# Performance work log

Hardware: AMD Instinct MI355X
Metric: run time of the kernel (lower is better)

## Reference

```python
import jax, jax.numpy as jnp
import numpy as np

N, S, D, H, L = 1024, 128, 128, 4, 2  # nodes, seq_len, d_model(=heads*C), heads, layers
C = D // H
EPS = 1e-5


def _bn(x, g, b):
    # torch BatchNorm1d training mode applied to [N, D, S]: per-channel stats over (node, seq)
    m = x.mean(axis=(0, 1))
    v = x.var(axis=(0, 1))  # biased variance, matching torch BN normalization
    return (x - m) * jax.lax.rsqrt(v + EPS) * g + b


def _ln(x, g, b):
    m = x.mean(-1, keepdims=True)
    v = x.var(-1, keepdims=True)
    return (x - m) * jax.lax.rsqrt(v + EPS) * g + b


def setup_inputs() -> dict:
    key = jax.random.key(0)
    ks = jax.random.split(key, 16)
    w = lambda k, shape: (jax.random.normal(k, shape, jnp.float32) * 0.05)
    x = jax.random.normal(ks[0], (N, S, D), jnp.float32)
    pad_mask = (jax.random.uniform(ks[1], (N, S, S)) > 0.2).astype(jnp.float32)
    ones = lambda shape: jnp.ones(shape, jnp.float32)
    zeros = lambda shape: jnp.zeros(shape, jnp.float32)
    inp = {
        'x': x, 'pad_mask': pad_mask,
        'lin_in_W': w(ks[2], (D, D)), 'lin_in_b': zeros((D,)),
        'in_bn_g': ones((D,)), 'in_bn_b': zeros((D,)),
        'q_W': w(ks[3], (L, D, D)), 'q_b': zeros((L, D)),
        'q_bn_g': ones((L, D)), 'q_bn_b': zeros((L, D)),
        'k_W': w(ks[4], (L, D, D)), 'k_b': zeros((L, D)),
        'k_bn_g': ones((L, D)), 'k_bn_b': zeros((L, D)),
        'v_W': w(ks[5], (L, D, D)), 'v_b': zeros((L, D)),
        'v_bn_g': ones((L, D)), 'v_bn_b': zeros((L, D)),
        'ln_g': ones((L, D)), 'ln_b': zeros((L, D)),
        'ff_W': w(ks[6], (L, D, D)), 'ff_b': zeros((L, D)),
        'ff_bn_g': ones((L, D)), 'ff_bn_b': zeros((L, D)),
        'skip_W': w(ks[7], (L, D, D)), 'skip_b': zeros((L, D)),
        'skip_bn_g': ones((L, D)), 'skip_bn_b': zeros((L, D)),
    }
    return inp


def reference(x, pad_mask, lin_in_W, lin_in_b, in_bn_g, in_bn_b,
              q_W, q_b, q_bn_g, q_bn_b, k_W, k_b, k_bn_g, k_bn_b,
              v_W, v_b, v_bn_g, v_bn_b, ln_g, ln_b,
              ff_W, ff_b, ff_bn_g, ff_bn_b, skip_W, skip_b, skip_bn_g, skip_bn_b):
    # DetourTransformer.forward: lin_in -> in_bn -> L DetourTransformerLayers -> take seq position 0
    h = _bn(x @ lin_in_W.T + lin_in_b, in_bn_g, in_bn_b)
    mask = pad_mask[:, None]  # [N,1,S,S], multiplicative mask applied BEFORE softmax
    for l in range(L):
        q = _bn(h @ q_W[l].T + q_b[l], q_bn_g[l], q_bn_b[l]).reshape(N, S, H, C)
        k = _bn(h @ k_W[l].T + k_b[l], k_bn_g[l], k_bn_b[l]).reshape(N, S, H, C)
        v = _bn(h @ v_W[l].T + v_b[l], v_bn_g[l], v_bn_b[l]).reshape(N, S, H, C)
        alpha = jnp.einsum('nshc,nthc->nhst', q, k) * mask  # no 1/sqrt(C) scaling in source
        attn = jax.nn.softmax(alpha, axis=-1)
        agg = jnp.einsum('nhst,nthc->nshc', attn, v).reshape(N, S, D)  # concat=True
        out = _ln(agg + h, ln_g[l], ln_b[l])
        ff = _bn(out @ ff_W[l].T + ff_b[l], ff_bn_g[l], ff_bn_b[l])
        out = _ln(out + ff, ln_g[l], ln_b[l])  # same shared LayerNorm params reused
        x_r = _bn(h @ skip_W[l].T + skip_b[l], skip_bn_g[l], skip_bn_b[l])
        h = out + x_r  # root_weight=True, beta=False
    return h[:, 0]
```

## Files before the change

kernel.cpp:

```cpp
#include <hip/hip_runtime.h>
#include <hip/hip_bf16.h>


typedef __attribute__((ext_vector_type(8))) short short8v;
typedef __attribute__((ext_vector_type(16))) float f32x16;

#define NBATCH 1024
#define SEQ    128
#define DIM    128
#define NLAYER 2
#define MTOT   (NBATCH*SEQ)
#define EPSF   1e-5f
#define INV_M  (1.0f/131072.0f)
#define HM32   ((long)MTOT * 32)

__device__ __forceinline__ float bf2f(ushort s) {
  return __uint_as_float(((uint)s) << 16);
}
__device__ __forceinline__ ushort f2bf(float f) {
  uint u = __float_as_uint(f);
  return (ushort)((u + 0x7FFFu + ((u >> 16) & 1u)) >> 16);
}

struct WPtrs { const float* p[11]; };

__global__ __launch_bounds__(256) void prep_w(WPtrs wp, ushort* __restrict__ dst)
{
  const int gid = blockIdx.x * 256 + threadIdx.x;
  const int m = gid >> 11;
  const int rem = gid & 2047;
  const int j = rem >> 4, kc = rem & 15;
  const float* src = wp.p[m];
  float4 a = *(const float4*)(src + j * DIM + kc * 8);
  float4 b = *(const float4*)(src + j * DIM + kc * 8 + 4);
  short8v v;
  v[0] = (short)f2bf(a.x); v[1] = (short)f2bf(a.y);
  v[2] = (short)f2bf(a.z); v[3] = (short)f2bf(a.w);
  v[4] = (short)f2bf(b.x); v[5] = (short)f2bf(b.y);
  v[6] = (short)f2bf(b.z); v[7] = (short)f2bf(b.w);
  const int nt = j >> 5, ln = j & 31;
  *(short8v*)(dst + m * 16384 + kc * 1024 + nt * 256 + ln * 8) = v;
}

__global__ __launch_bounds__(256) void pack_mask(
    const float* __restrict__ mask, uint4* __restrict__ mb)
{
  const int lane = threadIdx.x & 63;
  const int wv   = (blockIdx.x * 256 + threadIdx.x) >> 6;
  const int NW   = gridDim.x * 4;
  for (int row = wv; row < MTOT; row += NW) {
    const float a = mask[(long)row * SEQ + lane];
    const float b = mask[(long)row * SEQ + 64 + lane];
    const unsigned long long lo = __ballot(a != 0.f);
    const unsigned long long hi = __ballot(b != 0.f);
    if (lane == 0) {
      uint4 w;
      w.x = (uint)lo; w.y = (uint)(lo >> 32);
      w.z = (uint)hi; w.w = (uint)(hi >> 32);
      mb[row] = w;
    }
  }
}

template<int OM>
__global__ __launch_bounds__(256, 3) void gemm_one(
    const float* __restrict__ A, const ushort* __restrict__ Wm,
    float* __restrict__ outp, float* __restrict__ stats)
{
  __shared__ ushort Wl[16384];
  __shared__ float tb[4][1024];
  __shared__ float csum[128], csq[128];
  const int tid = threadIdx.x;
  const int lane = tid & 63, wid = tid >> 6;
  const int hi = lane >> 5, ln = lane & 31;
  const long m0 = (long)blockIdx.x * 128;
  const long arow = m0 + wid * 32 + ln;

#pragma unroll
  for (int i = 0; i < 8; ++i)
    ((short8v*)Wl)[i * 256 + tid] = ((const short8v*)Wm)[i * 256 + tid];

  if (tid < 128) { csum[tid] = 0.f; csq[tid] = 0.f; }

  short8v afr[8];
  {
    const float* ar = A + arow * DIM + hi * 8;
#pragma unroll
    for (int kt = 0; kt < 8; ++kt) {
      float4 a0 = *(const float4*)(ar + kt * 16);
      float4 a1 = *(const float4*)(ar + kt * 16 + 4);
      short8v v;
      v[0] = (short)f2bf(a0.x); v[1] = (short)f2bf(a0.y);
      v[2] = (short)f2bf(a0.z); v[3] = (short)f2bf(a0.w);
      v[4] = (short)f2bf(a1.x); v[5] = (short)f2bf(a1.y);
      v[6] = (short)f2bf(a1.z); v[7] = (short)f2bf(a1.w);
      afr[kt] = v;
    }
  }
  __syncthreads();

  f32x16 acc[4];
#pragma unroll
  for (int nt = 0; nt < 4; ++nt)
#pragma unroll
    for (int r = 0; r < 16; ++r) acc[nt][r] = 0.f;

#pragma unroll
  for (int kt = 0; kt < 8; ++kt) {
    const ushort* wb = Wl + (kt * 2 + hi) * 1024 + ln * 8;
#pragma unroll
    for (int nt = 0; nt < 4; ++nt) {
      short8v b = *(const short8v*)(wb + nt * 256);
      acc[nt] = __builtin_amdgcn_mfma_f32_32x32x16_bf16(afr[kt], b, acc[nt], 0, 0, 0);
    }
  }

  float ps[4], pq[4];
#pragma unroll
  for (int nt = 0; nt < 4; ++nt) { ps[nt] = 0.f; pq[nt] = 0.f; }

#pragma unroll
  for (int nt = 0; nt < 4; ++nt) {
#pragma unroll
    for (int r = 0; r < 16; ++r) {
      const float v = acc[nt][r];
      ps[nt] += v; pq[nt] += v * v;
      const int row = (r & 3) + 8 * (r >> 2) + 4 * hi;
      tb[wid][row * 32 + ln] = v;
    }
    if constexpr (OM == 0) {
#pragma unroll
      for (int i = 0; i < 4; ++i) {
        const int row = i * 8 + (lane >> 3);
        float4 v = *(const float4*)&tb[wid][row * 32 + (lane & 7) * 4];
        *(float4*)(outp + (m0 + wid * 32 + row) * DIM + nt * 32 + (lane & 7) * 4) = v;
      }
    } else {
      float* dst = outp + (long)nt * HM32 + (m0 + wid * 32) * 32;
#pragma unroll
      for (int i = 0; i < 4; ++i) {
        float4 v = *(const float4*)&tb[wid][i * 256 + lane * 4];
        *(float4*)(dst + i * 256 + lane * 4) = v;
      }
    }
  }

#pragma unroll
  for (int nt = 0; nt < 4; ++nt) {
    ps[nt] += __shfl_xor(ps[nt], 32);
    pq[nt] += __shfl_xor(pq[nt], 32);
  }
  __syncthreads();
  if (hi == 0) {
#pragma unroll
    for (int nt = 0; nt < 4; ++nt) {
      atomicAdd(&csum[nt * 32 + ln], ps[nt]);
      atomicAdd(&csq[nt * 32 + ln], pq[nt]);
    }
  }
  __syncthreads();
  if (tid < 128) {
    atomicAdd(&stats[tid],       csum[tid]);
    atomicAdd(&stats[128 + tid], csq[tid]);
  }
}

__global__ __launch_bounds__(256, 2) void gemm_qkvs(
    const float* __restrict__ A, const ushort* __restrict__ wbase,
    ushort* __restrict__ o0, ushort* __restrict__ o1,
    ushort* __restrict__ o2, ushort* __restrict__ o3,
    float* __restrict__ st0, float* __restrict__ st1,
    float* __restrict__ st2, float* __restrict__ st3)
{
  __shared__ ushort wbuf[2][16384];
  __shared__ ushort qtb[4][1024];
  __shared__ float csum[4][128], csq[4][128];
  const int tid = threadIdx.x;
  const int lane = tid & 63, wid = tid >> 6;
  const int hi = lane >> 5, ln = lane & 31;
  const long m0 = (long)blockIdx.x * 128;
  const long arow = m0 + wid * 32 + ln;

  if (tid < 128) {
#pragma unroll
    for (int w = 0; w < 4; ++w) { csum[w][tid] = 0.f; csq[w][tid] = 0.f; }
  }

  short8v afr[8];
  {
    const float* ar = A + arow * DIM + hi * 8;
#pragma unroll
    for (int kt = 0; kt < 8; ++kt) {
      float4 a0 = *(const float4*)(ar + kt * 16);
      float4 a1 = *(const float4*)(ar + kt * 16 + 4);
      short8v v;
      v[0] = (short)f2bf(a0.x); v[1] = (short)f2bf(a0.y);
      v[2] = (short)f2bf(a0.z); v[3] = (short)f2bf(a0.w);
      v[4] = (short)f2bf(a1.x); v[5] = (short)f2bf(a1.y);
      v[6] = (short)f2bf(a1.z); v[7] = (short)f2bf(a1.w);
      afr[kt] = v;
    }
  }

#pragma unroll
  for (int i = 0; i < 8; ++i)
    ((short8v*)wbuf[0])[i * 256 + tid] = ((const short8v*)wbase)[i * 256 + tid];

  float ps[4][4], pq[4][4];
#pragma unroll
  for (int w = 0; w < 4; ++w)
#pragma unroll
    for (int nt = 0; nt < 4; ++nt) { ps[w][nt] = 0.f; pq[w][nt] = 0.f; }

  __syncthreads();

#pragma unroll
  for (int w = 0; w < 4; ++w) {
    short8v nw[8];
    if (w < 3) {
      const int nxt = (w + 1 == 3) ? 4 : (w + 1);
      const short8v* src = (const short8v*)(wbase + nxt * 16384);
#pragma unroll
      for (int i = 0; i < 8; ++i) nw[i] = src[i * 256 + tid];
    }

    const ushort* wt = wbuf[w & 1];
    f32x16 acc[4];
#pragma unroll
    for (int nt = 0; nt < 4; ++nt)
#pragma unroll
      for (int r = 0; r < 16; ++r) acc[nt][r] = 0.f;
#pragma unroll
    for (int kt = 0; kt < 8; ++kt) {
      const ushort* wb = wt + (kt * 2 + hi) * 1024 + ln * 8;
#pragma unroll
      for (int nt = 0; nt < 4; ++nt) {
        short8v b = *(const short8v*)(wb + nt * 256);
        acc[nt] = __builtin_amdgcn_mfma_f32_32x32x16_bf16(afr[kt], b, acc[nt], 0, 0, 0);
      }
    }

    if (w < 3) {
      short8v* dst = (short8v*)wbuf[(w + 1) & 1];
#pragma unroll
      for (int i = 0; i < 8; ++i) dst[i * 256 + tid] = nw[i];
    }

    ushort* outp = (w == 0) ? o0 : (w == 1) ? o1 : (w == 2) ? o2 : o3;
#pragma unroll
    for (int nt = 0; nt < 4; ++nt) {
#pragma unroll
      for (int r = 0; r < 16; ++r) {
        const float v = acc[nt][r];
        ps[w][nt] += v; pq[w][nt] += v * v;
        const int row = (r & 3) + 8 * (r >> 2) + 4 * hi;
        qtb[wid][row * 32 + ln] = f2bf(v);
      }
      ushort* dst = outp + (long)nt * HM32 + (m0 + wid * 32) * 32;
      short8v v0 = *(const short8v*)&qtb[wid][lane * 8];
      short8v v1 = *(const short8v*)&qtb[wid][512 + lane * 8];
      *(short8v*)(dst + lane * 8)       = v0;
      *(short8v*)(dst + 512 + lane * 8) = v1;
    }
    __syncthreads();
  }

#pragma unroll
  for (int w = 0; w < 4; ++w) {
    float lps[4], lpq[4];
#pragma unroll
    for (int nt = 0; nt < 4; ++nt) {
      lps[nt] = ps[w][nt] + __shfl_xor(ps[w][nt], 32);
      lpq[nt] = pq[w][nt] + __shfl_xor(pq[w][nt], 32);
    }
    if (hi == 0) {
#pragma unroll
      for (int nt = 0; nt < 4; ++nt) {
        atomicAdd(&csum[w][nt * 32 + ln], lps[nt]);
        atomicAdd(&csq[w][nt * 32 + ln],  lpq[nt]);
      }
    }
  }
  __syncthreads();
  if (tid < 128) {
    atomicAdd(&st0[tid],       csum[0][tid]);
    atomicAdd(&st0[128 + tid], csq[0][tid]);
    atomicAdd(&st1[tid],       csum[1][tid]);
    atomicAdd(&st1[128 + tid], csq[1][tid]);
    atomicAdd(&st2[tid],       csum[2][tid]);
    atomicAdd(&st2[128 + tid], csq[2][tid]);
    atomicAdd(&st3[tid],       csum[3][tid]);
    atomicAdd(&st3[128 + tid], csq[3][tid]);
  }
}

__global__ __launch_bounds__(256) void bn_apply(
    float* __restrict__ x, const float* __restrict__ st,
    const float* __restrict__ g, const float* __restrict__ b)
{
  __shared__ float sc[128], bi[128];
  const int tid = threadIdx.x;
  if (tid < 128) {
    float mean = st[tid] * INV_M;
    float var  = st[128 + tid] * INV_M - mean * mean;
    float s = rsqrtf(var + EPSF) * g[tid];
    sc[tid] = s;
    bi[tid] = b[tid] - mean * s;
  }
  __syncthreads();
  const long total4 = (long)MTOT * DIM / 4;
  for (long i = (long)blockIdx.x * 256 + tid; i < total4; i += (long)gridDim.x * 256) {
    float4 vv = ((const float4*)x)[i];
    const int c = (int)((i * 4) & 127);
    vv.x = vv.x * sc[c + 0] + bi[c + 0];
    vv.y = vv.y * sc[c + 1] + bi[c + 1];
    vv.z = vv.z * sc[c + 2] + bi[c + 2];
    vv.w = vv.w * sc[c + 3] + bi[c + 3];
    ((float4*)x)[i] = vv;
  }
}

__global__ __launch_bounds__(256, 4) void attn_ln(
    const ushort* __restrict__ q, const ushort* __restrict__ k_in,
    const ushort* __restrict__ v_in,
    float* hbuf,
    const uint4* __restrict__ mb,
    const float* __restrict__ qst, const float* __restrict__ kst, const float* __restrict__ vst,
    const float* __restrict__ qg, const float* __restrict__ qbb,
    const float* __restrict__ kg, const float* __restrict__ kbb,
    const float* __restrict__ vg, const float* __restrict__ vbb,
    const float* __restrict__ lng, const float* __restrict__ lnb)
{
  __shared__ ushort Vp[128 * 136];
  __shared__ float qsc[128], qbi[128], ksc[128], kbi[128];
  __shared__ float reds[32][4], redq[32][4];
  __shared__ float2 rmv[32];

  const int tid = threadIdx.x;
  const int lane = tid & 63, hh = tid >> 6;
  const int hi = lane >> 5, ln = lane & 31;
  const int n = blockIdx.x;
  const long nb = (long)n * SEQ;
  const long hbase = (long)hh * HM32 + nb * 32;

  if (tid < 128) {
    const int c = tid;
    float m, v, s;
    m = qst[c] * INV_M; v = qst[128 + c] * INV_M - m * m;
    s = rsqrtf(v + EPSF) * qg[c];  qsc[c] = s; qbi[c] = qbb[c] - m * s;
    m = kst[c] * INV_M; v = kst[128 + c] * INV_M - m * m;
    s = rsqrtf(v + EPSF) * kg[c];  ksc[c] = s; kbi[c] = kbb[c] - m * s;
  }
  const int cg = hh * 32 + ln;
  float vs, vb0;
  {
    float m = vst[cg] * INV_M;
    float v = vst[128 + cg] * INV_M - m * m;
    vs = rsqrtf(v + EPSF) * vg[cg];
    vb0 = vbb[cg] - m * vs;
  }
  const float lgc = lng[cg], lbc = lnb[cg];

#pragma unroll
  for (int it = 0; it < 8; ++it) {
    const int t = it * 16 + (lane >> 2);
    const int c0 = (lane & 3) * 8;
    short8v vv = *(const short8v*)(v_in + hbase + (long)t * 32 + c0);
    const int tl = t & 31;
    const int kt = tl >> 4;
    const int rem = tl & 15;
    const int slot = (t & 96) + (kt << 4) + ((rem >> 2) & 1) * 8 + ((rem & 3) | (((rem >> 3) & 1) << 2));
#pragma unroll
    for (int i = 0; i < 8; ++i) Vp[(hh * 32 + c0 + i) * 136 + slot] = (ushort)vv[i];
  }
  __syncthreads();

  short8v kfr[4][2];
#pragma unroll
  for (int nt = 0; nt < 4; ++nt)
#pragma unroll
    for (int kt = 0; kt < 2; ++kt) {
      short8v raw = *(const short8v*)(k_in + hbase + (long)(nt * 32 + ln) * 32 + kt * 16 + hi * 8);
      short8v f;
#pragma unroll
      for (int i = 0; i < 8; ++i) {
        const int c = hh * 32 + kt * 16 + hi * 8 + i;
        f[i] = (short)f2bf(bf2f((ushort)raw[i]) * ksc[c] + kbi[c]);
      }
      kfr[nt][kt] = f;
    }

  for (int mt = 0; mt < 4; ++mt) {
    short8v qfr[2];
#pragma unroll
    for (int kt = 0; kt < 2; ++kt) {
      short8v raw = *(const short8v*)(q + hbase + (long)(mt * 32 + ln) * 32 + kt * 16 + hi * 8);
      short8v f;
#pragma unroll
      for (int i = 0; i < 8; ++i) {
        const int c = hh * 32 + kt * 16 + hi * 8 + i;
        f[i] = (short)f2bf(bf2f((ushort)raw[i]) * qsc[c] + qbi[c]);
      }
      qfr[kt] = f;
    }

    f32x16 st[4];
#pragma unroll
    for (int nt = 0; nt < 4; ++nt)
#pragma unroll
      for (int r = 0; r < 16; ++r) st[nt][r] = 0.f;
#pragma unroll
    for (int nt = 0; nt < 4; ++nt) {
      st[nt] = __builtin_amdgcn_mfma_f32_32x32x16_bf16(kfr[nt][0], qfr[0], st[nt], 0, 0, 0);
      st[nt] = __builtin_amdgcn_mfma_f32_32x32x16_bf16(kfr[nt][1], qfr[1], st[nt], 0, 0, 0);
    }

    const uint4 bw = mb[nb + mt * 32 + ln];
    float mx = -1e30f;
#pragma unroll
    for (int nt = 0; nt < 4; ++nt) {
      const uint word = (nt == 0) ? bw.x : (nt == 1) ? bw.y : (nt == 2) ? bw.z : bw.w;
#pragma unroll
      for (int r = 0; r < 16; ++r) {
        const int crow = (r & 3) + 8 * (r >> 2) + 4 * hi;
        st[nt][r] = ((word >> crow) & 1u) ? st[nt][r] : 0.f;
        mx = fmaxf(mx, st[nt][r]);
      }
    }
    mx = fmaxf(mx, __shfl_xor(mx, 32));
    float sum = 0.f;
#pragma unroll
    for (int nt = 0; nt < 4; ++nt)
#pragma unroll
      for (int r = 0; r < 16; ++r) {
        const float e = __expf(st[nt][r] - mx);
        st[nt][r] = e;
        sum += e;
      }
    sum += __shfl_xor(sum, 32);
    const float inv = 1.f / sum;

    f32x16 o;
#pragma unroll
    for (int r = 0; r < 16; ++r) o[r] = 0.f;
#pragma unroll
    for (int nt = 0; nt < 4; ++nt) {
#pragma unroll
      for (int kt = 0; kt < 2; ++kt) {
        short8v pa;
#pragma unroll
        for (int j = 0; j < 8; ++j) pa[j] = (short)f2bf(st[nt][kt * 8 + j] * inv);
        short8v vb = *(const short8v*)&Vp[(long)cg * 136 + nt * 32 + kt * 16 + hi * 8];
        o = __builtin_amdgcn_mfma_f32_32x32x16_bf16(pa, vb, o, 0, 0, 0);
      }
    }

    float yv[16];
#pragma unroll
    for (int r = 0; r < 16; ++r) {
      const int sl = (r & 3) + 8 * (r >> 2) + 4 * hi;
      const float hval = hbuf[(nb + mt * 32 + sl) * DIM + cg];
      yv[r] = vs * o[r] + vb0 + hval;
    }

#pragma unroll
    for (int r = 0; r < 16; ++r) {
      float s = yv[r], q2 = yv[r] * yv[r];
      s += __shfl_xor(s, 1);  q2 += __shfl_xor(q2, 1);
      s += __shfl_xor(s, 2);  q2 += __shfl_xor(q2, 2);
      s += __shfl_xor(s, 4);  q2 += __shfl_xor(q2, 4);
      s += __shfl_xor(s, 8);  q2 += __shfl_xor(q2, 8);
      s += __shfl_xor(s, 16); q2 += __shfl_xor(q2, 16);
      if (ln == 0) {
        const int sl = (r & 3) + 8 * (r >> 2) + 4 * hi;
        reds[sl][hh] = s; redq[sl][hh] = q2;
      }
    }
    __syncthreads();
    if (tid < 32) {
      const float s  = reds[tid][0] + reds[tid][1] + reds[tid][2] + reds[tid][3];
      const float q2 = redq[tid][0] + redq[tid][1] + redq[tid][2] + redq[tid][3];
      const float mean = s * (1.f / 128.f);
      const float var  = q2 * (1.f / 128.f) - mean * mean;
      rmv[tid] = make_float2(mean, rsqrtf(var + EPSF));
    }
    __syncthreads();
#pragma unroll
    for (int r = 0; r < 16; ++r) {
      const int sl = (r & 3) + 8 * (r >> 2) + 4 * hi;
      const float2 mr = rmv[sl];
      hbuf[(nb + mt * 32 + sl) * DIM + cg] = (yv[r] - mr.x) * mr.y * lgc + lbc;
    }
  }
}

template <bool FINAL>
__global__ __launch_bounds__(256) void fuse2_k(
    const float* t1, const float* __restrict__ ffr, const ushort* __restrict__ skr,
    const float* __restrict__ fst, const float* __restrict__ sst,
    const float* __restrict__ fg, const float* __restrict__ fb,
    const float* __restrict__ sg, const float* __restrict__ sb,
    const float* __restrict__ lg, const float* __restrict__ lb,
    float* out)
{
  const int lane = threadIdx.x & 63;
  const int c = lane * 2;
  float fs0, fbias0, fs1, fbias1, ss0, sbias0, ss1, sbias1;
  {
    float m0 = fst[c] * INV_M;
    float v0 = fst[128 + c] * INV_M - m0 * m0;
    fs0 = rsqrtf(v0 + EPSF) * fg[c];       fbias0 = fb[c] - m0 * fs0;
    float m1 = fst[c + 1] * INV_M;
    float v1 = fst[128 + c + 1] * INV_M - m1 * m1;
    fs1 = rsqrtf(v1 + EPSF) * fg[c + 1];   fbias1 = fb[c + 1] - m1 * fs1;
    float n0 = sst[c] * INV_M;
    float w0 = sst[128 + c] * INV_M - n0 * n0;
    ss0 = rsqrtf(w0 + EPSF) * sg[c];       sbias0 = sb[c] - n0 * ss0;
    float n1 = sst[c + 1] * INV_M;
    float w1 = sst[128 + c + 1] * INV_M - n1 * n1;
    ss1 = rsqrtf(w1 + EPSF) * sg[c + 1];   sbias1 = sb[c + 1] - n1 * ss1;
  }
  const float lg0 = lg[c], lg1 = lg[c + 1], lb0 = lb[c], lb1 = lb[c + 1];
  const int wid = (blockIdx.x * 256 + threadIdx.x) >> 6;
  const int NW  = gridDim.x * 4;
  const int ROWS = FINAL ? NBATCH : MTOT;
  const long thm = (long)(c >> 5) * HM32;
  for (int r = wid; r < ROWS; r += NW) {
    const long m   = FINAL ? (long)r * SEQ : (long)r;
    const long off = m * DIM + c;
    const long hm  = thm + m * 32 + (c & 31);
    float2 tv = *(const float2*)(t1 + off);
    float2 fv = *(const float2*)(ffr + hm);
    uint sv = *(const uint*)(skr + hm);
    float s0 = bf2f((ushort)(sv & 0xFFFFu)), s1 = bf2f((ushort)(sv >> 16));
    float y0 = tv.x + fv.x * fs0 + fbias0;
    float y1 = tv.y + fv.y * fs1 + fbias1;
    float s = y0 + y1, sq = y0 * y0 + y1 * y1;
#pragma unroll
    for (int o = 32; o; o >>= 1) { s += __shfl_xor(s, o); sq += __shfl_xor(sq, o); }
    const float mean = s * (1.f / 128.f);
    const float var  = sq * (1.f / 128.f) - mean * mean;
    const float rs   = rsqrtf(var + EPSF);
    float o0 = (y0 - mean) * rs * lg0 + lb0 + (s0 * ss0 + sbias0);
    float o1 = (y1 - mean) * rs * lg1 + lb1 + (s1 * ss1 + sbias1);
    const long ooff = FINAL ? ((long)r * DIM + c) : off;
    *(float2*)(out + ooff) = make_float2(o0, o1);
  }
}

extern "C" void kernel_launch(void* const* d_in, const int* in_sizes, int n_in,
                              void* d_out, int out_size, void* d_ws, size_t ws_size,
                              hipStream_t stream)
{
  (void)in_sizes; (void)n_in; (void)out_size; (void)ws_size;
  const float* x    = (const float*)d_in[0];
  const float* mask = (const float*)d_in[1];
  const float* linW = (const float*)d_in[2];
  const float* ing  = (const float*)d_in[4];
  const float* inb  = (const float*)d_in[5];
  const float* qW   = (const float*)d_in[6];
  const float* qg   = (const float*)d_in[8];
  const float* qb   = (const float*)d_in[9];
  const float* kW   = (const float*)d_in[10];
  const float* kg   = (const float*)d_in[12];
  const float* kb   = (const float*)d_in[13];
  const float* vW   = (const float*)d_in[14];
  const float* vg   = (const float*)d_in[16];
  const float* vb   = (const float*)d_in[17];
  const float* lng  = (const float*)d_in[18];
  const float* lnb  = (const float*)d_in[19];
  const float* ffW  = (const float*)d_in[20];
  const float* ffg  = (const float*)d_in[22];
  const float* ffb  = (const float*)d_in[23];
  const float* skW  = (const float*)d_in[24];
  const float* skg  = (const float*)d_in[26];
  const float* skb  = (const float*)d_in[27];

  const long MD = (long)MTOT * DIM;
  float*  stats = (float*)d_ws;
  float*  h     = (float*)d_ws + 4096;
  ushort* qbuf  = (ushort*)(h + MD);
  ushort* kbuf  = qbuf + MD;
  ushort* vbuf  = kbuf + MD;
  ushort* sbuf  = vbuf + MD;
  uint4*  mbits = (uint4*)(sbuf + MD);
  float*  ffbuf = (float*)qbuf;

  ushort* Wsw = (ushort*)d_out;
  hipMemsetAsync(stats, 0, 11 * 256 * sizeof(float), stream);

  WPtrs wp;
  wp.p[0] = linW;
  wp.p[1] = qW;            wp.p[2] = kW;            wp.p[3] = vW;
  wp.p[4] = ffW;           wp.p[5] = skW;
  wp.p[6] = qW + 16384;    wp.p[7] = kW + 16384;    wp.p[8] = vW + 16384;
  wp.p[9] = ffW + 16384;   wp.p[10] = skW + 16384;
  prep_w<<<88, 256, 0, stream>>>(wp, Wsw);
  pack_mask<<<512, 256, 0, stream>>>(mask, mbits);

  gemm_one<0><<<MTOT / 128, 256, 0, stream>>>(x, Wsw, h, stats);
  bn_apply<<<1024, 256, 0, stream>>>(h, stats, ing, inb);

  for (int l = 0; l < NLAYER; ++l) {
    const int poff = l * DIM;
    const ushort* wbase = Wsw + (1 + 5 * l) * 16384;
    float* stq = stats + (1 + 5 * l) * 256;
    float* stk = stats + (2 + 5 * l) * 256;
    float* stv = stats + (3 + 5 * l) * 256;
    float* stf = stats + (4 + 5 * l) * 256;
    float* sts = stats + (5 + 5 * l) * 256;

    gemm_qkvs<<<MTOT / 128, 256, 0, stream>>>(h, wbase, qbuf, kbuf, vbuf, sbuf,
                                              stq, stk, stv, sts);

    attn_ln<<<NBATCH, 256, 0, stream>>>(
        qbuf, kbuf, vbuf, h , mbits,
        stq, stk, stv,
        qg + poff, qb + poff, kg + poff, kb + poff, vg + poff, vb + poff,
        lng + poff, lnb + poff);

    gemm_one<1><<<MTOT / 128, 256, 0, stream>>>(
        h, wbase + 3 * 16384, ffbuf, stf);

    if (l < NLAYER - 1) {
      fuse2_k<false><<<1024, 256, 0, stream>>>(
          h, ffbuf, sbuf, stf, sts,
          ffg + poff, ffb + poff, skg + poff, skb + poff,
          lng + poff, lnb + poff, h );
    } else {
      fuse2_k<true><<<64, 256, 0, stream>>>(
          h, ffbuf, sbuf, stf, sts,
          ffg + poff, ffb + poff, skg + poff, skb + poff,
          lng + poff, lnb + poff, (float*)d_out);
    }
  }
}
```

Measured before the change: 514.0 us.

## Shrink LDS footprint of GEMM kernels to raise occupancy

Both projection GEMM kernels now use less shared memory. gemm_one stages its output in half-sized tiles and reuses the staging buffer for the column-stat reduction. gemm_qkvs streams each weight matrix in two K-halves through a smaller double buffer, and its stats scratch aliases the output staging buffer. Launch bounds are raised to 4 blocks per SM to allow more resident waves and better latency hiding. The cost is extra barriers and smaller prefetch chunks, and the higher bound may cap registers and cause spilling.

```diff
diff --git a/kernel.cpp b/kernel.cpp
--- a/kernel.cpp
+++ b/kernel.cpp
@@ -63,13 +63,12 @@
 }
 
 template<int OM>
-__global__ __launch_bounds__(256, 3) void gemm_one(
+__global__ __launch_bounds__(256, 4) void gemm_one(
     const float* __restrict__ A, const ushort* __restrict__ Wm,
     float* __restrict__ outp, float* __restrict__ stats)
 {
   __shared__ ushort Wl[16384];
-  __shared__ float tb[4][1024];
-  __shared__ float csum[128], csq[128];
+  __shared__ float tb[4][512];
   const int tid = threadIdx.x;
   const int lane = tid & 63, wid = tid >> 6;
   const int hi = lane >> 5, ln = lane & 31;
@@ -79,8 +78,6 @@
 #pragma unroll
   for (int i = 0; i < 8; ++i)
     ((short8v*)Wl)[i * 256 + tid] = ((const short8v*)Wm)[i * 256 + tid];
-
-  if (tid < 128) { csum[tid] = 0.f; csq[tid] = 0.f; }
 
   short8v afr[8];
   {
@@ -122,25 +119,29 @@
 #pragma unroll
   for (int nt = 0; nt < 4; ++nt) {
 #pragma unroll
-    for (int r = 0; r < 16; ++r) {
-      const float v = acc[nt][r];
-      ps[nt] += v; pq[nt] += v * v;
-      const int row = (r & 3) + 8 * (r >> 2) + 4 * hi;
-      tb[wid][row * 32 + ln] = v;
-    }
-    if constexpr (OM == 0) {
-#pragma unroll
-      for (int i = 0; i < 4; ++i) {
-        const int row = i * 8 + (lane >> 3);
-        float4 v = *(const float4*)&tb[wid][row * 32 + (lane & 7) * 4];
-        *(float4*)(outp + (m0 + wid * 32 + row) * DIM + nt * 32 + (lane & 7) * 4) = v;
-      }
-    } else {
-      float* dst = outp + (long)nt * HM32 + (m0 + wid * 32) * 32;
-#pragma unroll
-      for (int i = 0; i < 4; ++i) {
-        float4 v = *(const float4*)&tb[wid][i * 256 + lane * 4];
-        *(float4*)(dst + i * 256 + lane * 4) = v;
+    for (int h2 = 0; h2 < 2; ++h2) {
+#pragma unroll
+      for (int rr = 0; rr < 8; ++rr) {
+        const int r = h2 * 8 + rr;
+        const float v = acc[nt][r];
+        ps[nt] += v; pq[nt] += v * v;
+        const int lrow = (rr & 3) + 8 * (rr >> 2) + 4 * hi;
+        tb[wid][lrow * 32 + ln] = v;
+      }
+      if constexpr (OM == 0) {
+#pragma unroll
+        for (int i = 0; i < 2; ++i) {
+          const int lrow = i * 8 + (lane >> 3);
+          float4 v = *(const float4*)&tb[wid][lrow * 32 + (lane & 7) * 4];
+          *(float4*)(outp + (m0 + wid * 32 + h2 * 16 + lrow) * DIM + nt * 32 + (lane & 7) * 4) = v;
+        }
+      } else {
+        float* dst = outp + (long)nt * HM32 + (m0 + wid * 32 + h2 * 16) * 32;
+#pragma unroll
+        for (int i = 0; i < 2; ++i) {
+          float4 v = *(const float4*)&tb[wid][i * 256 + lane * 4];
+          *(float4*)(dst + i * 256 + lane * 4) = v;
+        }
       }
     }
   }
@@ -150,41 +151,38 @@
     ps[nt] += __shfl_xor(ps[nt], 32);
     pq[nt] += __shfl_xor(pq[nt], 32);
   }
+  float* cs = (float*)tb;
+  __syncthreads();
+  if (tid < 256) cs[tid] = 0.f;
   __syncthreads();
   if (hi == 0) {
 #pragma unroll
     for (int nt = 0; nt < 4; ++nt) {
-      atomicAdd(&csum[nt * 32 + ln], ps[nt]);
-      atomicAdd(&csq[nt * 32 + ln], pq[nt]);
+      atomicAdd(&cs[nt * 32 + ln], ps[nt]);
+      atomicAdd(&cs[128 + nt * 32 + ln], pq[nt]);
     }
   }
   __syncthreads();
   if (tid < 128) {
-    atomicAdd(&stats[tid],       csum[tid]);
-    atomicAdd(&stats[128 + tid], csq[tid]);
-  }
-}
-
-__global__ __launch_bounds__(256, 2) void gemm_qkvs(
+    atomicAdd(&stats[tid],       cs[tid]);
+    atomicAdd(&stats[128 + tid], cs[128 + tid]);
+  }
+}
+
+__global__ __launch_bounds__(256, 4) void gemm_qkvs(
     const float* __restrict__ A, const ushort* __restrict__ wbase,
     ushort* __restrict__ o0, ushort* __restrict__ o1,
     ushort* __restrict__ o2, ushort* __restrict__ o3,
     float* __restrict__ st0, float* __restrict__ st1,
     float* __restrict__ st2, float* __restrict__ st3)
 {
-  __shared__ ushort wbuf[2][16384];
+  __shared__ ushort wbuf[2][8192];
   __shared__ ushort qtb[4][1024];
-  __shared__ float csum[4][128], csq[4][128];
   const int tid = threadIdx.x;
   const int lane = tid & 63, wid = tid >> 6;
   const int hi = lane >> 5, ln = lane & 31;
   const long m0 = (long)blockIdx.x * 128;
   const long arow = m0 + wid * 32 + ln;
-
-  if (tid < 128) {
-#pragma unroll
-    for (int w = 0; w < 4; ++w) { csum[w][tid] = 0.f; csq[w][tid] = 0.f; }
-  }
 
   short8v afr[8];
   {
@@ -203,7 +201,7 @@
   }
 
 #pragma unroll
-  for (int i = 0; i < 8; ++i)
+  for (int i = 0; i < 4; ++i)
     ((short8v*)wbuf[0])[i * 256 + tid] = ((const short8v*)wbase)[i * 256 + tid];
 
   float ps[4][4], pq[4][4];
@@ -212,27 +210,35 @@
 #pragma unroll
     for (int nt = 0; nt < 4; ++nt) { ps[w][nt] = 0.f; pq[w][nt] = 0.f; }
 
-  __syncthreads();
-
-#pragma unroll
-  for (int w = 0; w < 4; ++w) {
-    short8v nw[8];
-    if (w < 3) {
-      const int nxt = (w + 1 == 3) ? 4 : (w + 1);
-      const short8v* src = (const short8v*)(wbase + nxt * 16384);
-#pragma unroll
-      for (int i = 0; i < 8; ++i) nw[i] = src[i * 256 + tid];
-    }
-
-    const ushort* wt = wbuf[w & 1];
-    f32x16 acc[4];
-#pragma unroll
-    for (int nt = 0; nt < 4; ++nt)
-#pragma unroll
-      for (int r = 0; r < 16; ++r) acc[nt][r] = 0.f;
-#pragma unroll
-    for (int kt = 0; kt < 8; ++kt) {
-      const ushort* wb = wt + (kt * 2 + hi) * 1024 + ln * 8;
+  f32x16 acc[4];
+  __syncthreads();
+
+  const int wofl[4] = {0, 1, 2, 4};
+
+#pragma unroll
+  for (int s = 0; s < 8; ++s) {
+    const int w = s >> 1, half = s & 1;
+
+    short8v nw[4];
+    if (s < 7) {
+      const int ns = s + 1;
+      const short8v* src = (const short8v*)(wbase + wofl[ns >> 1] * 16384 + (ns & 1) * 8192);
+#pragma unroll
+      for (int i = 0; i < 4; ++i) nw[i] = src[i * 256 + tid];
+    }
+
+    if (half == 0) {
+#pragma unroll
+      for (int nt = 0; nt < 4; ++nt)
+#pragma unroll
+        for (int r = 0; r < 16; ++r) acc[nt][r] = 0.f;
+    }
+
+    const ushort* wt = wbuf[s & 1];
+#pragma unroll
+    for (int ktl = 0; ktl < 4; ++ktl) {
+      const int kt = half * 4 + ktl;
+      const ushort* wb = wt + (ktl * 2 + hi) * 1024 + ln * 8;
 #pragma unroll
       for (int nt = 0; nt < 4; ++nt) {
         short8v b = *(const short8v*)(wb + nt * 256);
@@ -240,31 +246,36 @@
       }
     }
 
-    if (w < 3) {
-      short8v* dst = (short8v*)wbuf[(w + 1) & 1];
-#pragma unroll
-      for (int i = 0; i < 8; ++i) dst[i * 256 + tid] = nw[i];
-    }
-
-    ushort* outp = (w == 0) ? o0 : (w == 1) ? o1 : (w == 2) ? o2 : o3;
-#pragma unroll
-    for (int nt = 0; nt < 4; ++nt) {
-#pragma unroll
-      for (int r = 0; r < 16; ++r) {
-        const float v = acc[nt][r];
-        ps[w][nt] += v; pq[w][nt] += v * v;
-        const int row = (r & 3) + 8 * (r >> 2) + 4 * hi;
-        qtb[wid][row * 32 + ln] = f2bf(v);
-      }
-      ushort* dst = outp + (long)nt * HM32 + (m0 + wid * 32) * 32;
-      short8v v0 = *(const short8v*)&qtb[wid][lane * 8];
-      short8v v1 = *(const short8v*)&qtb[wid][512 + lane * 8];
-      *(short8v*)(dst + lane * 8)       = v0;
-      *(short8v*)(dst + 512 + lane * 8) = v1;
+    if (s < 7) {
+      short8v* dst = (short8v*)wbuf[(s + 1) & 1];
+#pragma unroll
+      for (int i = 0; i < 4; ++i) dst[i * 256 + tid] = nw[i];
+    }
+
+    if (half == 1) {
+      ushort* outp = (w == 0) ? o0 : (w == 1) ? o1 : (w == 2) ? o2 : o3;
+#pragma unroll
+      for (int nt = 0; nt < 4; ++nt) {
+#pragma unroll
+        for (int r = 0; r < 16; ++r) {
+          const float v = acc[nt][r];
+          ps[w][nt] += v; pq[w][nt] += v * v;
+          const int row = (r & 3) + 8 * (r >> 2) + 4 * hi;
+          qtb[wid][row * 32 + ln] = f2bf(v);
+        }
+        ushort* dst = outp + (long)nt * HM32 + (m0 + wid * 32) * 32;
+        short8v v0 = *(const short8v*)&qtb[wid][lane * 8];
+        short8v v1 = *(const short8v*)&qtb[wid][512 + lane * 8];
+        *(short8v*)(dst + lane * 8)       = v0;
+        *(short8v*)(dst + 512 + lane * 8) = v1;
+      }
     }
     __syncthreads();
   }
 
+  float* cs = (float*)qtb;
+  cs[tid] = 0.f; cs[256 + tid] = 0.f; cs[512 + tid] = 0.f; cs[768 + tid] = 0.f;
+  __syncthreads();
 #pragma unroll
   for (int w = 0; w < 4; ++w) {
     float lps[4], lpq[4];
@@ -276,21 +287,21 @@
     if (hi == 0) {
 #pragma unroll
       for (int nt = 0; nt < 4; ++nt) {
-        atomicAdd(&csum[w][nt * 32 + ln], lps[nt]);
-        atomicAdd(&csq[w][nt * 32 + ln],  lpq[nt]);
+        atomicAdd(&cs[w * 256 + nt * 32 + ln], lps[nt]);
+        atomicAdd(&cs[w * 256 + 128 + nt * 32 + ln], lpq[nt]);
       }
     }
   }
   __syncthreads();
   if (tid < 128) {
-    atomicAdd(&st0[tid],       csum[0][tid]);
-    atomicAdd(&st0[128 + tid], csq[0][tid]);
-    atomicAdd(&st1[tid],       csum[1][tid]);
-    atomicAdd(&st1[128 + tid], csq[1][tid]);
-    atomicAdd(&st2[tid],       csum[2][tid]);
-    atomicAdd(&st2[128 + tid], csq[2][tid]);
-    atomicAdd(&st3[tid],       csum[3][tid]);
-    atomicAdd(&st3[128 + tid], csq[3][tid]);
+    atomicAdd(&st0[tid],       cs[tid]);
+    atomicAdd(&st0[128 + tid], cs[128 + tid]);
+    atomicAdd(&st1[tid],       cs[256 + tid]);
+    atomicAdd(&st1[128 + tid], cs[384 + tid]);
+    atomicAdd(&st2[tid],       cs[512 + tid]);
+    atomicAdd(&st2[128 + tid], cs[640 + tid]);
+    atomicAdd(&st3[tid],       cs[768 + tid]);
+    atomicAdd(&st3[128 + tid], cs[896 + tid]);
   }
 }
 
```

Result: slower. 671.3 us (+30.6%).
